# Performance work log

Measured on AMD Instinct MI355X. Metric: run time of the kernel, lower is better.

## Reference

```python
import jax, jax.numpy as jnp
import numpy as np

B, S, E, H = 8, 2048, 1024, 64

def setup_inputs() -> dict:
    key = jax.random.key(0)
    ks = jax.random.split(key, 7)
    scale = 1.0 / np.sqrt(E)
    return {
        "x": jax.random.normal(ks[0], (B, S, E), dtype=jnp.float32),
        "mask": jnp.ones((B, S), dtype=jnp.int32),
        "Wq": jax.random.uniform(ks[1], (E, H), jnp.float32, -scale, scale),
        "bq": jax.random.uniform(ks[2], (H,), jnp.float32, -scale, scale),
        "Wk": jax.random.uniform(ks[3], (E, H), jnp.float32, -scale, scale),
        "bk": jax.random.uniform(ks[4], (H,), jnp.float32, -scale, scale),
        "Wv": jax.random.uniform(ks[5], (E, H), jnp.float32, -scale, scale),
        "bv": jax.random.uniform(ks[6], (H,), jnp.float32, -scale, scale),
    }

def reference(x, mask, Wq, bq, Wk, bk, Wv, bv):
    # q,k,v: [B,S,H]
    q = jnp.einsum('bse,eh->bsh', x, Wq) + bq
    k = jnp.einsum('bse,eh->bsh', x, Wk) + bk
    v = jnp.einsum('bse,eh->bsh', x, Wv) + bv
    # scores: [B,S,S]
    scores = jnp.einsum('bqh,bkh->bqk', q, k) / jnp.sqrt(jnp.asarray(H, q.dtype))
    causal = jnp.tril(jnp.ones((S, S), dtype=bool))  # [S,S]
    pad = (mask != 0)[:, None, :]                    # [B,1,S]
    neg_inf = jnp.asarray(float('-inf'), scores.dtype)
    scores = jnp.where(causal[None] & pad, scores, neg_inf)
    attn = jax.nn.softmax(scores, axis=-1)
    return jnp.einsum('bqk,bkh->bqh', attn, v)
```

## Files before the change

kernel.cpp:

```cpp
#include <hip/hip_runtime.h>
#include <hip/hip_bf16.h>

#define S_ 2048
#define E_ 1024
#define QNC 16

typedef __attribute__((ext_vector_type(8))) short short8;
typedef __attribute__((ext_vector_type(4))) float f32x4;

__device__ __forceinline__ short f2bf(float f) {
    __hip_bfloat16 h = __float2bfloat16(f);
    return *(short*)&h;
}

__device__ __forceinline__ void g2l16(const void* g, void* l) {
    __builtin_amdgcn_global_load_lds(
        (const __attribute__((address_space(1))) void*)g,
        (__attribute__((address_space(3))) void*)l, 16, 0, 0);
}

__global__ __launch_bounds__(256) void prep_weights(
    const float* __restrict__ Wq, const float* __restrict__ Wk,
    const float* __restrict__ Wv, unsigned short* __restrict__ Wtt)
{
    int tw = blockIdx.x * 256 + threadIdx.x;
    int nt = tw >> 11;
    int lane = tw & 63;
    int n = nt * 16 + (lane & 15);
    int h = n & 63;
    const float* W = (n < 64) ? Wq : (n < 128) ? Wk : Wv;
    int k0 = ((tw >> 6) & 31) * 32 + (lane >> 4) * 8;
    short8 o;
    #pragma unroll
    for (int e = 0; e < 8; ++e) o[e] = f2bf(W[(k0 + e) * 64 + h]);
    *(short8*)(Wtt + (size_t)tw * 8) = o;
}

__global__ __launch_bounds__(256, 4) void qkv_main(
    const float* __restrict__ x, const unsigned short* __restrict__ Wtt,
    const float* __restrict__ bq, const float* __restrict__ bk,
    const float* __restrict__ bv,
    unsigned short* __restrict__ Q, unsigned short* __restrict__ K,
    unsigned short* __restrict__ Vt)
{
    __shared__ __align__(16) char lds[5][4096];
    __shared__ __align__(16) char eq[16 * 272];
    __shared__ __align__(16) unsigned short ev[64 * 18];
    int tid = threadIdx.x;
    int wave = tid >> 6, lane = tid & 63;
    int lo = lane & 15, hi = lane >> 4;
    int wn = wave;
    int rowbase = blockIdx.x * 16;
    const char* xg = (const char*)x;

    f32x4 acc[3];
    #pragma unroll
    for (int j = 0; j < 3; ++j) acc[j] = (f32x4){0.f, 0.f, 0.f, 0.f};

    #define STAGE(bb, kc)                                                         \
        {                                                                         \
            int r_ = tid >> 4, u_ = tid & 15;                                     \
            const char* src = xg + (size_t)(rowbase + r_) * 4096 + (kc) * 256     \
                              + (((u_ & 8) | ((u_ & 7) ^ (r_ & 7))) << 4);        \
            g2l16(src, &lds[bb][wave * 1024]);                                    \
        }

    #define LOADB(dst, t)                                                         \
        {                                                                         \
            _Pragma("unroll")                                                     \
            for (int j = 0; j < 3; ++j)                                           \
                _Pragma("unroll")                                                 \
                for (int kk = 0; kk < 2; ++kk)                                    \
                    dst[j][kk] = *(const short8*)(Wtt +                           \
                        (size_t)(((wn * 3 + j) * 32 + (t) * 2 + kk) * 64 + lane) * 8); \
        }

    #define COMPUTE(bfr, t)                                                       \
        {                                                                         \
            const char* lx = lds[(t) % 5];                                        \
            _Pragma("unroll")                                                     \
            for (int kk = 0; kk < 2; ++kk) {                                      \
                int u0 = kk * 8 + hi * 2;                                         \
                float4 a0 = *(const float4*)(lx + lo * 256                        \
                    + (((u0 & 8) | ((u0 & 7) ^ (lo & 7))) << 4));                 \
                float4 a1 = *(const float4*)(lx + lo * 256                        \
                    + ((((u0 + 1) & 8) | (((u0 + 1) & 7) ^ (lo & 7))) << 4));     \
                short8 af;                                                        \
                af[0] = f2bf(a0.x); af[1] = f2bf(a0.y);                           \
                af[2] = f2bf(a0.z); af[3] = f2bf(a0.w);                           \
                af[4] = f2bf(a1.x); af[5] = f2bf(a1.y);                           \
                af[6] = f2bf(a1.z); af[7] = f2bf(a1.w);                           \
                _Pragma("unroll")                                                 \
                for (int j = 0; j < 3; ++j)                                       \
                    acc[j] = __builtin_amdgcn_mfma_f32_16x16x32_bf16(             \
                        af, bfr[j][kk], acc[j], 0, 0, 0);                         \
            }                                                                     \
        }

    #define WAITQ(t)                                                              \
        {                                                                         \
            if ((t) <= 11)      asm volatile("s_waitcnt vmcnt(8)" ::: "memory");  \
            else if ((t) <= 13) asm volatile("s_waitcnt vmcnt(6)" ::: "memory");  \
            else                asm volatile("s_waitcnt vmcnt(0)" ::: "memory");  \
        }

    short8 bfrA[3][2], bfrB[3][2];

    LOADB(bfrA, 0);
    __builtin_amdgcn_sched_barrier(0);
    STAGE(0, 0); STAGE(1, 1); STAGE(2, 2); STAGE(3, 3);
    __builtin_amdgcn_sched_barrier(0);
    asm volatile("s_waitcnt vmcnt(3)" ::: "memory");
    __builtin_amdgcn_sched_barrier(0);
    __builtin_amdgcn_s_barrier();

    for (int tb = 0; tb < 8; ++tb) {
        int t0 = 2 * tb, t1 = 2 * tb + 1;
        LOADB(bfrB, t1);
        COMPUTE(bfrA, t0);
        if (t0 + 4 < QNC) STAGE((t0 + 4) % 5, t0 + 4);
        __builtin_amdgcn_sched_barrier(0);
        WAITQ(t0);
        __builtin_amdgcn_sched_barrier(0);
        __builtin_amdgcn_s_barrier();

        if (t1 + 1 < QNC) LOADB(bfrA, t1 + 1);
        COMPUTE(bfrB, t1);
        if (t1 + 4 < QNC) STAGE((t1 + 4) % 5, t1 + 4);
        if (t1 < QNC - 1) {
            __builtin_amdgcn_sched_barrier(0);
            WAITQ(t1);
            __builtin_amdgcn_sched_barrier(0);
            __builtin_amdgcn_s_barrier();
        }
    }
    #undef STAGE
    #undef LOADB
    #undef COMPUTE
    #undef WAITQ

    __syncthreads();
    #pragma unroll
    for (int j = 0; j < 3; ++j) {
        int n = wn * 48 + j * 16 + lo;
        #pragma unroll
        for (int r = 0; r < 4; ++r) {
            int rr = 4 * hi + r;
            float v = acc[j][r];
            if (n < 64) {
                *(unsigned short*)(eq + rr * 272 + n * 2) =
                    (unsigned short)f2bf(v + bq[n]);
            } else if (n < 128) {
                *(unsigned short*)(eq + rr * 272 + n * 2) =
                    (unsigned short)f2bf(v + bk[n - 64]);
            } else {
                ev[(n - 128) * 18 + rr] = (unsigned short)f2bf(v + bv[n - 128]);
            }
        }
    }
    __syncthreads();

    {
        int row = tid >> 4, seg = tid & 15;
        short8 val = *(const short8*)(eq + row * 272 + seg * 16);
        if (seg < 8)
            *(short8*)(Q + (size_t)(rowbase + row) * 64 + seg * 8) = val;
        else
            *(short8*)(K + (size_t)(rowbase + row) * 64 + (seg - 8) * 8) = val;
    }
    if (tid < 128) {
        int h = tid >> 1, su = tid & 1;
        int b = rowbase >> 11, sl0 = rowbase & (S_ - 1);
        short8 val = *(const short8*)((const char*)ev + h * 36 + su * 16);
        *(short8*)(Vt + ((size_t)(b * 64 + h)) * S_ + sl0 + su * 8) = val;
    }
}

__global__ __launch_bounds__(256) void attn_stage(
    const unsigned short* __restrict__ Q, const unsigned short* __restrict__ K,
    const unsigned short* __restrict__ Vt, const int* __restrict__ mask,
    float* __restrict__ part)
{
    __shared__ __align__(16) char kv[3][16384];
    __shared__ __align__(16) unsigned short p_lds[4][16][72];
    int tid = threadIdx.x;
    int wave = tid >> 6, lane = tid & 63;
    int lo = lane & 15, hi = lane >> 4;
    int blk = blockIdx.x;
    int c = blk & 3;
    int pr = blk >> 2;
    int b = pr & 7;
    int qt64 = 31 - (pr >> 3);
    int nkt = qt64 + 1;
    int chunk = (nkt + 3) >> 2;
    int kt0 = c * chunk;
    int kt1 = min(kt0 + chunk, nkt);
    int ntile = kt1 - kt0;
    int qrow0 = qt64 * 64 + wave * 16;

    f32x4 o[4];
    float ps[4] = {0.f, 0.f, 0.f, 0.f};
    #pragma unroll
    for (int i = 0; i < 4; ++i) o[i] = (f32x4){0.f, 0.f, 0.f, 0.f};

    #define ASTAGE(bb, kt)                                                        \
        {                                                                         \
            int kbase_ = (kt) * 64;                                               \
            const char* kg = (const char*)K + (size_t)(b * S_ + kbase_) * 128;    \
            const char* vg = (const char*)Vt + (size_t)b * 64 * 4096 + kbase_ * 2;\
            _Pragma("unroll")                                                     \
            for (int j = 0; j < 2; ++j) {                                         \
                int r = (j * 4 + wave) * 8 + (lane >> 3);                         \
                int un = lane & 7;                                                \
                g2l16(kg + r * 128 + ((un ^ (r & 7)) << 4),                       \
                      &kv[bb][(j * 4 + wave) * 1024]);                            \
                g2l16(vg + (size_t)r * 4096 + ((un ^ (r & 7)) << 4),              \
                      &kv[bb][8192 + (j * 4 + wave) * 1024]);                     \
            }                                                                     \
        }

    if (ntile > 0) {
        const unsigned short* qp = Q + ((size_t)(b * S_ + qrow0 + lo)) * 64 + 8 * hi;
        short8 qf0 = *(const short8*)(qp);
        short8 qf1 = *(const short8*)(qp + 32);

        unsigned mbits = 0;
        for (int tt = 0; tt < 8; ++tt) {
            if (tt < ntile) {
                int kbase = (kt0 + tt) * 64;
                #pragma unroll
                for (int nt = 0; nt < 4; ++nt)
                    if (mask[b * S_ + kbase + nt * 16 + lo] != 0)
                        mbits |= (1u << (tt * 4 + nt));
            }
        }
        asm volatile("s_waitcnt vmcnt(0)" ::: "memory");
        __builtin_amdgcn_sched_barrier(0);

        ASTAGE(0, kt0);
        if (ntile > 1) ASTAGE(1, kt0 + 1);
        __builtin_amdgcn_sched_barrier(0);
        if (ntile > 1) asm volatile("s_waitcnt vmcnt(4)" ::: "memory");
        else           asm volatile("s_waitcnt vmcnt(0)" ::: "memory");
        __builtin_amdgcn_sched_barrier(0);
        __builtin_amdgcn_s_barrier();

        for (int t = 0; t < ntile; ++t) {
            int kbase = (kt0 + t) * 64;
            const char* kb = kv[t % 3];
            const char* vb = kv[t % 3] + 8192;

            f32x4 s[4];
            #pragma unroll
            for (int i = 0; i < 4; ++i) s[i] = (f32x4){0.f, 0.f, 0.f, 0.f};
            #pragma unroll
            for (int nt = 0; nt < 4; ++nt) {
                short8 kf0 = *(const short8*)(kb + (nt * 16 + lo) * 128 + ((hi ^ (lo & 7)) << 4));
                short8 kf1 = *(const short8*)(kb + (nt * 16 + lo) * 128 + (((4 + hi) ^ (lo & 7)) << 4));
                s[nt] = __builtin_amdgcn_mfma_f32_16x16x32_bf16(qf0, kf0, s[nt], 0, 0, 0);
                s[nt] = __builtin_amdgcn_mfma_f32_16x16x32_bf16(qf1, kf1, s[nt], 0, 0, 0);
            }

            #pragma unroll
            for (int nt = 0; nt < 4; ++nt) {
                int kpos = kbase + nt * 16 + lo;
                bool mok = (mbits >> (t * 4 + nt)) & 1;
                #pragma unroll
                for (int r = 0; r < 4; ++r) {
                    int qpos = qrow0 + 4 * hi + r;
                    bool ok = mok && (kpos <= qpos);
                    float pv = ok ? __expf(s[nt][r] * 0.125f) : 0.f;
                    ps[r] += pv;
                    p_lds[wave][4 * hi + r][nt * 16 + lo] = (unsigned short)f2bf(pv);
                }
            }

            #pragma unroll
            for (int kk = 0; kk < 2; ++kk) {
                short8 pf = *(const short8*)&p_lds[wave][lo][kk * 32 + 8 * hi];
                #pragma unroll
                for (int nt = 0; nt < 4; ++nt) {
                    short8 vf = *(const short8*)(vb + (nt * 16 + lo) * 128
                                                 + (((kk * 4 + hi) ^ (lo & 7)) << 4));
                    o[nt] = __builtin_amdgcn_mfma_f32_16x16x32_bf16(pf, vf, o[nt], 0, 0, 0);
                }
            }

            if (t + 2 < ntile) ASTAGE((t + 2) % 3, kt0 + t + 2);
            __builtin_amdgcn_sched_barrier(0);
            if (t + 1 < ntile) {
                if (t + 2 < ntile) asm volatile("s_waitcnt vmcnt(4)" ::: "memory");
                else               asm volatile("s_waitcnt vmcnt(0)" ::: "memory");
                __builtin_amdgcn_sched_barrier(0);
                __builtin_amdgcn_s_barrier();
            }
        }
    }
    #undef ASTAGE

    float l[4];
    #pragma unroll
    for (int r = 0; r < 4; ++r) {
        float v = ps[r];
        v += __shfl_xor(v, 1);
        v += __shfl_xor(v, 2);
        v += __shfl_xor(v, 4);
        v += __shfl_xor(v, 8);
        l[r] = v;
    }

    int tile16 = b * 128 + qt64 * 4 + wave;
    float* pp = part + (((size_t)c * 1024 + tile16) * 64 + lane) * 20;
    #pragma unroll
    for (int nt = 0; nt < 4; ++nt) *(f32x4*)(pp + nt * 4) = o[nt];
    f32x4 ll;
    #pragma unroll
    for (int r = 0; r < 4; ++r) ll[r] = l[r];
    *(f32x4*)(pp + 16) = ll;
}

__global__ __launch_bounds__(256) void attn_comb(
    const float* __restrict__ part, float* __restrict__ out)
{
    int g = blockIdx.x * 256 + threadIdx.x;
    int tile = g >> 6, lane = g & 63;
    int lo = lane & 15, hi = lane >> 4;
    int b = tile >> 7, qt = tile & 127;
    int qrow0 = qt * 16;

    f32x4 o[4];
    float l[4] = {0.f, 0.f, 0.f, 0.f};
    #pragma unroll
    for (int i = 0; i < 4; ++i) o[i] = (f32x4){0.f, 0.f, 0.f, 0.f};

    #pragma unroll
    for (int c = 0; c < 4; ++c) {
        const float* pp = part + (((size_t)c * 1024 + tile) * 64 + lane) * 20;
        #pragma unroll
        for (int nt = 0; nt < 4; ++nt) {
            f32x4 po = *(const f32x4*)(pp + nt * 4);
            #pragma unroll
            for (int r = 0; r < 4; ++r) o[nt][r] += po[r];
        }
        f32x4 pl = *(const f32x4*)(pp + 16);
        #pragma unroll
        for (int r = 0; r < 4; ++r) l[r] += pl[r];
    }

    #pragma unroll
    for (int nt = 0; nt < 4; ++nt) {
        #pragma unroll
        for (int r = 0; r < 4; ++r) {
            int qpos = qrow0 + 4 * hi + r;
            out[((size_t)(b * S_ + qpos)) * 64 + nt * 16 + lo] =
                (l[r] > 0.f) ? o[nt][r] / l[r] : 0.f;
        }
    }
}

extern "C" void kernel_launch(void* const* d_in, const int* in_sizes, int n_in,
                              void* d_out, int out_size, void* d_ws, size_t ws_size,
                              hipStream_t stream) {
    const float* x   = (const float*)d_in[0];
    const int*   msk = (const int*)d_in[1];
    const float* Wq  = (const float*)d_in[2];
    const float* bq  = (const float*)d_in[3];
    const float* Wk  = (const float*)d_in[4];
    const float* bk  = (const float*)d_in[5];
    const float* Wv  = (const float*)d_in[6];
    const float* bv  = (const float*)d_in[7];
    float* outp = (float*)d_out;

    char* w = (char*)d_ws;
    unsigned short* Wtt = (unsigned short*)w;
    unsigned short* Qb = (unsigned short*)(w + 0x080000);
    unsigned short* Kb = (unsigned short*)(w + 0x280000);
    unsigned short* Vt = (unsigned short*)(w + 0x480000);
    float* partp = (float*)(w + 0x680000);

    prep_weights<<<dim3(96), dim3(256), 0, stream>>>(Wq, Wk, Wv, Wtt);
    qkv_main<<<dim3(1024), dim3(256), 0, stream>>>(x, Wtt, bq, bk, bv, Qb, Kb, Vt);
    attn_stage<<<dim3(1024), dim3(256), 0, stream>>>(Qb, Kb, Vt, msk, partp);
    attn_comb<<<dim3(256), dim3(256), 0, stream>>>(partp, outp);
}
```

Baseline: 61.14 us.

## Stage weights through LDS with 32-row tiles and double-buffered QKV projection

The QKV projection kernel now handles 32 rows per block instead of 16, with a 2x2 wave layout. Both the x tile and the bf16 weight chunk are staged into a double-buffered LDS pool via global_load_lds, replacing per-wave direct global loads of pre-swizzled weight fragments. prep_weights now writes a plain transposed [n][k] bf16 layout. Larger tiles halve how often weights are re-read per row, but pipeline depth drops from 4 stages to 2, and the larger LDS footprint lowers occupancy (launch bound 2).

```diff
diff --git a/kernel.cpp b/kernel.cpp
--- a/kernel.cpp
+++ b/kernel.cpp
@@ -21,132 +21,102 @@
 
 __global__ __launch_bounds__(256) void prep_weights(
     const float* __restrict__ Wq, const float* __restrict__ Wk,
-    const float* __restrict__ Wv, unsigned short* __restrict__ Wtt)
+    const float* __restrict__ Wv, unsigned short* __restrict__ Wt)
 {
-    int tw = blockIdx.x * 256 + threadIdx.x;
-    int nt = tw >> 11;
-    int lane = tw & 63;
-    int n = nt * 16 + (lane & 15);
-    int h = n & 63;
+    int idx = blockIdx.x * 256 + threadIdx.x;
+    int n = idx >> 10, k = idx & (E_ - 1);
     const float* W = (n < 64) ? Wq : (n < 128) ? Wk : Wv;
-    int k0 = ((tw >> 6) & 31) * 32 + (lane >> 4) * 8;
-    short8 o;
-    #pragma unroll
-    for (int e = 0; e < 8; ++e) o[e] = f2bf(W[(k0 + e) * 64 + h]);
-    *(short8*)(Wtt + (size_t)tw * 8) = o;
-}
-
-__global__ __launch_bounds__(256, 4) void qkv_main(
-    const float* __restrict__ x, const unsigned short* __restrict__ Wtt,
+    Wt[idx] = (unsigned short)f2bf(W[k * 64 + (n & 63)]);
+}
+
+__global__ __launch_bounds__(256, 2) void qkv_main(
+    const float* __restrict__ x, const unsigned short* __restrict__ Wt,
     const float* __restrict__ bq, const float* __restrict__ bk,
     const float* __restrict__ bv,
     unsigned short* __restrict__ Q, unsigned short* __restrict__ K,
     unsigned short* __restrict__ Vt)
 {
-    __shared__ __align__(16) char lds[5][4096];
-    __shared__ __align__(16) char eq[16 * 272];
-    __shared__ __align__(16) unsigned short ev[64 * 18];
+    __shared__ __align__(16) char pool[2][32768];
     int tid = threadIdx.x;
     int wave = tid >> 6, lane = tid & 63;
     int lo = lane & 15, hi = lane >> 4;
-    int wn = wave;
-    int rowbase = blockIdx.x * 16;
+    int wm = wave >> 1, wn = wave & 1;
+    int rowbase = blockIdx.x * 32;
     const char* xg = (const char*)x;
-
-    f32x4 acc[3];
-    #pragma unroll
-    for (int j = 0; j < 3; ++j) acc[j] = (f32x4){0.f, 0.f, 0.f, 0.f};
+    const char* wg = (const char*)Wt;
+
+    f32x4 acc[6];
+    #pragma unroll
+    for (int j = 0; j < 6; ++j) acc[j] = (f32x4){0.f, 0.f, 0.f, 0.f};
 
     #define STAGE(bb, kc)                                                         \
         {                                                                         \
-            int r_ = tid >> 4, u_ = tid & 15;                                     \
-            const char* src = xg + (size_t)(rowbase + r_) * 4096 + (kc) * 256     \
-                              + (((u_ & 8) | ((u_ & 7) ^ (r_ & 7))) << 4);        \
-            g2l16(src, &lds[bb][wave * 1024]);                                    \
-        }
-
-    #define LOADB(dst, t)                                                         \
-        {                                                                         \
             _Pragma("unroll")                                                     \
-            for (int j = 0; j < 3; ++j)                                           \
-                _Pragma("unroll")                                                 \
-                for (int kk = 0; kk < 2; ++kk)                                    \
-                    dst[j][kk] = *(const short8*)(Wtt +                           \
-                        (size_t)(((wn * 3 + j) * 32 + (t) * 2 + kk) * 64 + lane) * 8); \
-        }
-
-    #define COMPUTE(bfr, t)                                                       \
-        {                                                                         \
-            const char* lx = lds[(t) % 5];                                        \
+            for (int i = 0; i < 2; ++i) {                                         \
+                int u_lin = i * 256 + tid;                                        \
+                int r = u_lin >> 4, u = u_lin & 15;                               \
+                const char* src = xg + (size_t)(rowbase + r) * 4096 + (kc) * 256  \
+                                  + (((u & 8) | ((u & 7) ^ (r & 7))) << 4);       \
+                g2l16(src, &pool[bb][(i * 256 + wave * 64) * 16]);                \
+            }                                                                     \
             _Pragma("unroll")                                                     \
-            for (int kk = 0; kk < 2; ++kk) {                                      \
-                int u0 = kk * 8 + hi * 2;                                         \
-                float4 a0 = *(const float4*)(lx + lo * 256                        \
-                    + (((u0 & 8) | ((u0 & 7) ^ (lo & 7))) << 4));                 \
-                float4 a1 = *(const float4*)(lx + lo * 256                        \
-                    + ((((u0 + 1) & 8) | (((u0 + 1) & 7) ^ (lo & 7))) << 4));     \
-                short8 af;                                                        \
-                af[0] = f2bf(a0.x); af[1] = f2bf(a0.y);                           \
-                af[2] = f2bf(a0.z); af[3] = f2bf(a0.w);                           \
-                af[4] = f2bf(a1.x); af[5] = f2bf(a1.y);                           \
-                af[6] = f2bf(a1.z); af[7] = f2bf(a1.w);                           \
-                _Pragma("unroll")                                                 \
-                for (int j = 0; j < 3; ++j)                                       \
-                    acc[j] = __builtin_amdgcn_mfma_f32_16x16x32_bf16(             \
-                        af, bfr[j][kk], acc[j], 0, 0, 0);                         \
+            for (int i = 0; i < 6; ++i) {                                         \
+                int u_lin = i * 256 + tid;                                        \
+                int c = u_lin >> 3, u = u_lin & 7;                                \
+                const char* src = wg + (size_t)c * 2048 + (kc) * 128              \
+                                  + ((u ^ (c & 7)) << 4);                         \
+                g2l16(src, &pool[bb][8192 + (i * 256 + wave * 64) * 16]);         \
             }                                                                     \
         }
 
-    #define WAITQ(t)                                                              \
-        {                                                                         \
-            if ((t) <= 11)      asm volatile("s_waitcnt vmcnt(8)" ::: "memory");  \
-            else if ((t) <= 13) asm volatile("s_waitcnt vmcnt(6)" ::: "memory");  \
-            else                asm volatile("s_waitcnt vmcnt(0)" ::: "memory");  \
-        }
-
-    short8 bfrA[3][2], bfrB[3][2];
-
-    LOADB(bfrA, 0);
-    __builtin_amdgcn_sched_barrier(0);
-    STAGE(0, 0); STAGE(1, 1); STAGE(2, 2); STAGE(3, 3);
-    __builtin_amdgcn_sched_barrier(0);
-    asm volatile("s_waitcnt vmcnt(3)" ::: "memory");
+    STAGE(0, 0);
+    asm volatile("s_waitcnt vmcnt(0)" ::: "memory");
     __builtin_amdgcn_sched_barrier(0);
     __builtin_amdgcn_s_barrier();
 
-    for (int tb = 0; tb < 8; ++tb) {
-        int t0 = 2 * tb, t1 = 2 * tb + 1;
-        LOADB(bfrB, t1);
-        COMPUTE(bfrA, t0);
-        if (t0 + 4 < QNC) STAGE((t0 + 4) % 5, t0 + 4);
-        __builtin_amdgcn_sched_barrier(0);
-        WAITQ(t0);
+    for (int t = 0; t < QNC; ++t) {
+        if (t + 1 < QNC) STAGE((t + 1) & 1, t + 1);
+
+        const char* lx = pool[t & 1];
+        const char* lw = pool[t & 1] + 8192;
+        int r = wm * 16 + lo;
+        #pragma unroll
+        for (int kk = 0; kk < 2; ++kk) {
+            int u0 = kk * 8 + hi * 2;
+            float4 a0 = *(const float4*)(lx + r * 256
+                + (((u0 & 8) | ((u0 & 7) ^ (r & 7))) << 4));
+            float4 a1 = *(const float4*)(lx + r * 256
+                + ((((u0 + 1) & 8) | (((u0 + 1) & 7) ^ (r & 7))) << 4));
+            short8 af;
+            af[0] = f2bf(a0.x); af[1] = f2bf(a0.y);
+            af[2] = f2bf(a0.z); af[3] = f2bf(a0.w);
+            af[4] = f2bf(a1.x); af[5] = f2bf(a1.y);
+            af[6] = f2bf(a1.z); af[7] = f2bf(a1.w);
+            #pragma unroll
+            for (int j = 0; j < 6; ++j) {
+                int c = wn * 96 + j * 16 + lo;
+                short8 bf = *(const short8*)(lw + c * 128
+                    + (((kk * 4 + hi) ^ (c & 7)) << 4));
+                acc[j] = __builtin_amdgcn_mfma_f32_16x16x32_bf16(af, bf, acc[j], 0, 0, 0);
+            }
+        }
+
+        __builtin_amdgcn_sched_barrier(0);
+        asm volatile("s_waitcnt vmcnt(0)" ::: "memory");
         __builtin_amdgcn_sched_barrier(0);
         __builtin_amdgcn_s_barrier();
-
-        if (t1 + 1 < QNC) LOADB(bfrA, t1 + 1);
-        COMPUTE(bfrB, t1);
-        if (t1 + 4 < QNC) STAGE((t1 + 4) % 5, t1 + 4);
-        if (t1 < QNC - 1) {
-            __builtin_amdgcn_sched_barrier(0);
-            WAITQ(t1);
-            __builtin_amdgcn_sched_barrier(0);
-            __builtin_amdgcn_s_barrier();
-        }
     }
     #undef STAGE
-    #undef LOADB
-    #undef COMPUTE
-    #undef WAITQ
-
-    __syncthreads();
-    #pragma unroll
-    for (int j = 0; j < 3; ++j) {
-        int n = wn * 48 + j * 16 + lo;
-        #pragma unroll
-        for (int r = 0; r < 4; ++r) {
-            int rr = 4 * hi + r;
-            float v = acc[j][r];
+
+    char* eq = pool[0];
+    unsigned short* ev = (unsigned short*)pool[1];
+    #pragma unroll
+    for (int j = 0; j < 6; ++j) {
+        int n = wn * 96 + j * 16 + lo;
+        #pragma unroll
+        for (int rr4 = 0; rr4 < 4; ++rr4) {
+            int rr = wm * 16 + 4 * hi + rr4;
+            float v = acc[j][rr4];
             if (n < 64) {
                 *(unsigned short*)(eq + rr * 272 + n * 2) =
                     (unsigned short)f2bf(v + bq[n]);
@@ -154,24 +124,26 @@
                 *(unsigned short*)(eq + rr * 272 + n * 2) =
                     (unsigned short)f2bf(v + bk[n - 64]);
             } else {
-                ev[(n - 128) * 18 + rr] = (unsigned short)f2bf(v + bv[n - 128]);
+                ev[(n - 128) * 40 + rr] = (unsigned short)f2bf(v + bv[n - 128]);
             }
         }
     }
     __syncthreads();
 
     {
-        int row = tid >> 4, seg = tid & 15;
-        short8 val = *(const short8*)(eq + row * 272 + seg * 16);
-        if (seg < 8)
-            *(short8*)(Q + (size_t)(rowbase + row) * 64 + seg * 8) = val;
-        else
-            *(short8*)(K + (size_t)(rowbase + row) * 64 + (seg - 8) * 8) = val;
-    }
-    if (tid < 128) {
-        int h = tid >> 1, su = tid & 1;
+        #pragma unroll
+        for (int i = 0; i < 2; ++i) {
+            int u_lin = i * 256 + tid;
+            int row = u_lin >> 4, seg = u_lin & 15;
+            short8 val = *(const short8*)(eq + row * 272 + seg * 16);
+            if (seg < 8)
+                *(short8*)(Q + (size_t)(rowbase + row) * 64 + seg * 8) = val;
+            else
+                *(short8*)(K + (size_t)(rowbase + row) * 64 + (seg - 8) * 8) = val;
+        }
+        int h = tid >> 2, su = tid & 3;
         int b = rowbase >> 11, sl0 = rowbase & (S_ - 1);
-        short8 val = *(const short8*)((const char*)ev + h * 36 + su * 16);
+        short8 val = *(const short8*)(ev + h * 40 + su * 8);
         *(short8*)(Vt + ((size_t)(b * 64 + h)) * S_ + sl0 + su * 8) = val;
     }
 }
@@ -372,14 +344,14 @@
     float* outp = (float*)d_out;
 
     char* w = (char*)d_ws;
-    unsigned short* Wtt = (unsigned short*)w;
+    unsigned short* Wt = (unsigned short*)w;
     unsigned short* Qb = (unsigned short*)(w + 0x080000);
     unsigned short* Kb = (unsigned short*)(w + 0x280000);
     unsigned short* Vt = (unsigned short*)(w + 0x480000);
     float* partp = (float*)(w + 0x680000);
 
-    prep_weights<<<dim3(96), dim3(256), 0, stream>>>(Wq, Wk, Wv, Wtt);
-    qkv_main<<<dim3(1024), dim3(256), 0, stream>>>(x, Wtt, bq, bk, bv, Qb, Kb, Vt);
+    prep_weights<<<dim3(768), dim3(256), 0, stream>>>(Wq, Wk, Wv, Wt);
+    qkv_main<<<dim3(512), dim3(256), 0, stream>>>(x, Wt, bq, bk, bv, Qb, Kb, Vt);
     attn_stage<<<dim3(1024), dim3(256), 0, stream>>>(Qb, Kb, Vt, msk, partp);
     attn_comb<<<dim3(256), dim3(256), 0, stream>>>(partp, outp);
 }
```

Measured after the change: 58.32 us. 1.05x faster.
